# Optimization experiments

Hardware: AMD Instinct MI355X
Metric: run time of the kernel (lower is better)

Reference implementation:

```python
import jax, jax.numpy as jnp
import numpy as np

C1, CS = 512, 32
EPS = 1e-5
_HI, _HJ = np.triu_indices(CS, k=1)  # pairwise (i<j) hadamard index pairs, cs_expand = 496


def setup_inputs() -> dict:
    key = jax.random.key(0)
    ks = jax.random.split(key, 9)
    B, H, W = 16, 32, 32
    return dict(
        x=jax.random.normal(ks[0], (B, C1, H, W), jnp.float32),
        fc_w=jax.random.normal(ks[1], (C1, C1), jnp.float32) * 0.05,   # 1x1 conv kernel
        fc_b=jax.random.normal(ks[2], (C1,), jnp.float32) * 0.05,
        bn_gamma=jax.random.normal(ks[3], (C1,), jnp.float32) * 0.1 + 1.0,
        bn_beta=jax.random.normal(ks[4], (C1,), jnp.float32) * 0.1,
        bn_mean=jax.random.normal(ks[5], (C1,), jnp.float32) * 0.1,    # BN running mean
        bn_var=jax.random.uniform(ks[6], (C1,), jnp.float32) + 0.5,    # BN running var (positive)
        eva_w=jax.random.normal(ks[7], (C1, C1), jnp.float32) * 0.05,
        eva_b=jax.random.normal(ks[8], (C1,), jnp.float32) * 0.05,
    )


def reference(x, fc_w, fc_b, bn_gamma, bn_beta, bn_mean, bn_var, eva_w, eva_b):
    hi = jnp.asarray(_HI)
    hj = jnp.asarray(_HJ)
    # 1x1 conv (pointwise GEMM over channels)
    x = jnp.einsum('bchw,oc->bohw', x, fc_w) + fc_b[None, :, None, None]
    # BatchNorm2d, eval mode (running stats)
    scale = bn_gamma / jnp.sqrt(bn_var + EPS)
    x = (x - bn_mean[None, :, None, None]) * scale[None, :, None, None] + bn_beta[None, :, None, None]
    # channel evaluation logits: global avg pool -> linear
    logits = jnp.mean(x, axis=(2, 3)) @ eva_w.T + eva_b  # [B, C1]
    # top-cs channel selection and gather (eval path)
    _, idx = jax.lax.top_k(logits, CS)                    # [B, CS]
    x_sel = jax.vmap(lambda xi, ii: xi[ii])(x, idx)       # [B, CS, H, W]
    # pairwise hadamard expansion: gather-multiply over (i<j) pairs
    prod = x_sel[:, hi] * x_sel[:, hj]                    # [B, cs_expand, H, W]
    # CrossHadaNorm: per-channel standardize with batch stats, affine from
    # cross-products of norm_x affine params gathered via hadamard_i/j
    mean = jnp.mean(prod, axis=(0, 2, 3), keepdims=True)
    var = jnp.var(prod, axis=(0, 2, 3), keepdims=True)
    g = (bn_gamma[hi] * bn_gamma[hj])[None, :, None, None]
    b = (bn_beta[hi] * bn_beta[hj])[None, :, None, None]
    prod = (prod - mean) / jnp.sqrt(var + EPS) * g + b
    return jnp.concatenate([x, prod], axis=1)             # [B, c1 + cs_expand, H, W]
```

## Files before the change

kernel.cpp:

```cpp
#include <hip/hip_runtime.h>
#include <stdint.h>
#include <stddef.h>

#define B_   16
#define C1_  512
#define HW_  1024
#define CS_  32
#define CE_  496
#define CO_  1008

typedef __attribute__((ext_vector_type(8))) short short8;
typedef __attribute__((ext_vector_type(4))) short short4v;
typedef __attribute__((ext_vector_type(4))) float f32x4;

__device__ __forceinline__ short f2bf(float f) {
  unsigned u = __builtin_bit_cast(unsigned, f);
  unsigned r = (u + 0x7fffu + ((u >> 16) & 1u)) >> 16;
  return (short)(unsigned short)r;
}

__device__ __forceinline__ void gload_lds16(const void* g, void* l) {
  __builtin_amdgcn_global_load_lds(
      (const __attribute__((address_space(1))) unsigned int*)g,
      (__attribute__((address_space(3))) unsigned int*)l, 16, 0, 0);
}

__global__ __launch_bounds__(256) void prep_kernel(
    const float* __restrict__ fc_w, const float* __restrict__ fc_b,
    const float* __restrict__ bn_gamma, const float* __restrict__ bn_beta,
    const float* __restrict__ bn_mean, const float* __restrict__ bn_var,
    short* __restrict__ wbf, float* __restrict__ bs, float* __restrict__ bb) {
  int bid = blockIdx.x, tid = threadIdx.x;
  if (bid < 1024) {
    int i = bid * 256 + tid;
    wbf[i] = f2bf(fc_w[i]);
  } else {
    for (int o = tid; o < C1_; o += 256) {
      float s = bn_gamma[o] / sqrtf(bn_var[o] + 1e-5f);
      bs[o] = s;
      bb[o] = (fc_b[o] - bn_mean[o]) * s + bn_beta[o];
    }
  }
}

__global__ __launch_bounds__(256) void transpose_pool(const float* __restrict__ x,
                                                      short* __restrict__ xT,
                                                      float* __restrict__ partial) {
  __shared__ float tile[64][65];
  int bid = blockIdx.x;
  int b = bid >> 7;
  int tt = bid & 127;
  int ct = tt >> 4, pt = tt & 15;
  int c0 = ct * 64, p0 = pt * 64;
  int tid = threadIdx.x;
  int rr = tid >> 4, lc = tid & 15;
  const float* xb = x + (size_t)b * C1_ * HW_;
#pragma unroll
  for (int it = 0; it < 4; ++it) {
    int c = it * 16 + rr;
    int p4 = lc * 4;
    float4 v = *(const float4*)(xb + (size_t)(c0 + c) * HW_ + p0 + p4);
    tile[c][p4+0] = v.x; tile[c][p4+1] = v.y; tile[c][p4+2] = v.z; tile[c][p4+3] = v.w;
    float g = v.x + v.y + v.z + v.w;
    g += __shfl_down(g, 8, 16);
    g += __shfl_down(g, 4, 16);
    g += __shfl_down(g, 2, 16);
    g += __shfl_down(g, 1, 16);
    if (lc == 0) partial[((size_t)b * 16 + pt) * C1_ + c0 + c] = g;
  }
  __syncthreads();
#pragma unroll
  for (int it = 0; it < 4; ++it) {
    int p = it * 16 + rr;
    int c4 = lc * 4;
    short4v o;
    o[0] = f2bf(tile[c4+0][p]);
    o[1] = f2bf(tile[c4+1][p]);
    o[2] = f2bf(tile[c4+2][p]);
    o[3] = f2bf(tile[c4+3][p]);
    *(short4v*)(xT + (size_t)b * HW_ * C1_ + (size_t)(p0 + p) * C1_ + c0 + c4) = o;
  }
}

__global__ __launch_bounds__(64) void fc_pool_kernel(
    const float* __restrict__ partial, const float* __restrict__ fc_w,
    const float* __restrict__ bs, const float* __restrict__ bb,
    float* __restrict__ pb) {
  int b = blockIdx.x >> 3, ot = blockIdx.x & 7;
  int tid = threadIdx.x;
  __shared__ float px[512];
  for (int c = tid; c < 512; c += 64) {
    float s = 0.f;
#pragma unroll
    for (int pt = 0; pt < 16; ++pt) s += partial[((size_t)b * 16 + pt) * C1_ + c];
    px[c] = s * (1.f / 1024.f);
  }
  __syncthreads();
  int o = ot * 64 + tid;
  const float4* wr = (const float4*)(fc_w + (size_t)o * 512);
  float acc = 0.f;
#pragma unroll 8
  for (int q = 0; q < 128; ++q) {
    float4 w = wr[q];
    acc += w.x * px[q*4] + w.y * px[q*4+1] + w.z * px[q*4+2] + w.w * px[q*4+3];
  }
  pb[b * 512 + o] = acc * bs[o] + bb[o];
}

__global__ __launch_bounds__(64) void eva_kernel(
    const float* __restrict__ pb, const float* __restrict__ eva_w,
    const float* __restrict__ eva_b, float* __restrict__ logits) {
  int b = blockIdx.x >> 3, ot = blockIdx.x & 7;
  int tid = threadIdx.x;
  __shared__ float ps[512];
  for (int c = tid; c < 512; c += 64) ps[c] = pb[b * 512 + c];
  __syncthreads();
  int o = ot * 64 + tid;
  const float4* wr = (const float4*)(eva_w + (size_t)o * 512);
  float acc = 0.f;
#pragma unroll 8
  for (int q = 0; q < 128; ++q) {
    float4 w = wr[q];
    acc += w.x * ps[q*4] + w.y * ps[q*4+1] + w.z * ps[q*4+2] + w.w * ps[q*4+3];
  }
  logits[b * 512 + o] = acc + eva_b[o];
}

__global__ __launch_bounds__(64) void topk_kernel(const float* __restrict__ logits,
                                                  int* __restrict__ idx) {
  int b = blockIdx.x, lane = threadIdx.x;
  float v[8];
  int base = lane * 8;
#pragma unroll
  for (int u = 0; u < 8; ++u) v[u] = logits[b * 512 + base + u];
  for (int it = 0; it < CS_; ++it) {
    float bv = v[0]; int bu = 0;
#pragma unroll
    for (int u = 1; u < 8; ++u) if (v[u] > bv) { bv = v[u]; bu = u; }
    int bi = base + bu;
    for (int off = 32; off; off >>= 1) {
      float ov = __shfl_down(bv, off);
      int   oi = __shfl_down(bi, off);
      if (ov > bv || (ov == bv && oi < bi)) { bv = ov; bi = oi; }
    }
    bi = __shfl(bi, 0);
    if (lane == 0) idx[b * CS_ + it] = bi;
#pragma unroll
    for (int u = 0; u < 8; ++u) if (bi == base + u) v[u] = -3.4e38f;
  }
}

__global__ __launch_bounds__(256) void gemm_kernel(const short* __restrict__ W,
                                                   const short* __restrict__ XT,
                                                   const float* __restrict__ bs,
                                                   const float* __restrict__ bb,
                                                   float* __restrict__ out) {
  __shared__ short As[2][128 * 32];
  __shared__ short Bs[2][128 * 32];
  int bid = (blockIdx.x & 7) * 64 + (blockIdx.x >> 3);
  int b = bid >> 5;
  int t = bid & 31;
  int mt = t & 3, ntile = t >> 2;
  int m0 = mt * 128, n0 = ntile * 128;
  const short* Ag = W + (size_t)m0 * 512;
  const short* Bg = XT + (size_t)b * HW_ * 512 + (size_t)n0 * 512;
  int tid = threadIdx.x;
  int lane = tid & 63, wave = tid >> 6;
  int wr = wave >> 1, wc = wave & 1;
  int mrow = wr * 64, ncol = wc * 64;
  int lrow = lane & 15;
  int lk = (lane >> 4) * 8;

  f32x4 acc[4][4];
#pragma unroll
  for (int i = 0; i < 4; ++i)
#pragma unroll
    for (int j = 0; j < 4; ++j) acc[i][j] = (f32x4){0.f, 0.f, 0.f, 0.f};

#pragma unroll
  for (int it = 0; it < 2; ++it) {
    int s = it * 256 + tid;
    int r = s >> 2, q = s & 3;
    gload_lds16(Ag + (size_t)r * 512 + q * 8, &As[0][s * 8]);
    gload_lds16(Bg + (size_t)r * 512 + q * 8, &Bs[0][s * 8]);
  }
  asm volatile("s_waitcnt vmcnt(0)" ::: "memory");
  __syncthreads();

  int cur = 0;
  for (int kt = 0; kt < 16; ++kt) {
    if (kt < 15) {
      int k0 = (kt + 1) * 32;
#pragma unroll
      for (int it = 0; it < 2; ++it) {
        int s = it * 256 + tid;
        int r = s >> 2, q = s & 3;
        gload_lds16(Ag + (size_t)r * 512 + k0 + q * 8, &As[cur ^ 1][s * 8]);
        gload_lds16(Bg + (size_t)r * 512 + k0 + q * 8, &Bs[cur ^ 1][s * 8]);
      }
    }
    short8 af[4], bfv[4];
#pragma unroll
    for (int f = 0; f < 4; ++f) {
      af[f]  = *(const short8*)(&As[cur][(mrow + f * 16 + lrow) * 32 + lk]);
      bfv[f] = *(const short8*)(&Bs[cur][(ncol + f * 16 + lrow) * 32 + lk]);
    }
#pragma unroll
    for (int mf = 0; mf < 4; ++mf)
#pragma unroll
      for (int nf = 0; nf < 4; ++nf)
        acc[mf][nf] = __builtin_amdgcn_mfma_f32_16x16x32_bf16(af[mf], bfv[nf], acc[mf][nf], 0, 0, 0);
    asm volatile("s_waitcnt vmcnt(0)" ::: "memory");
    __syncthreads();
    cur ^= 1;
  }

  float* outb = out + (size_t)b * CO_ * HW_;
#pragma unroll
  for (int mf = 0; mf < 4; ++mf) {
#pragma unroll
    for (int j = 0; j < 4; ++j) {
      int o = m0 + mrow + mf * 16 + (lane >> 4) * 4 + j;
      float s = bs[o], bv = bb[o];
#pragma unroll
      for (int nf = 0; nf < 4; ++nf) {
        int p = n0 + ncol + nf * 16 + lrow;
        outb[(size_t)o * HW_ + p] = acc[mf][nf][j] * s + bv;
      }
    }
  }
}

__global__ __launch_bounds__(256) void hada_kernel(
    const int* __restrict__ idx, const float* __restrict__ bn_gamma,
    const float* __restrict__ bn_beta, float* __restrict__ out) {
  int e = blockIdx.x, tid = threadIdx.x;
  int lane = tid & 63, wave = tid >> 6;
  int i = 0, rem = e;
  while (rem >= 31 - i) { rem -= 31 - i; ++i; }
  int j = i + 1 + rem;

  __shared__ int chi[16], chj[16];
  if (tid < 16) chi[tid] = idx[tid * CS_ + i];
  else if (tid < 32) chj[tid - 16] = idx[(tid - 16) * CS_ + j];
  __syncthreads();

  f32x4 p[16];
  float s = 0.f, s2 = 0.f;
#pragma unroll
  for (int b = 0; b < 16; ++b) {
    const float4* xi = (const float4*)(out + ((size_t)b * CO_ + chi[b]) * HW_);
    const float4* xj = (const float4*)(out + ((size_t)b * CO_ + chj[b]) * HW_);
    float4 a = xi[tid], c = xj[tid];
    p[b][0] = a.x * c.x; p[b][1] = a.y * c.y; p[b][2] = a.z * c.z; p[b][3] = a.w * c.w;
    s  += p[b][0] + p[b][1] + p[b][2] + p[b][3];
    s2 += p[b][0]*p[b][0] + p[b][1]*p[b][1] + p[b][2]*p[b][2] + p[b][3]*p[b][3];
  }
  for (int off = 32; off; off >>= 1) { s += __shfl_down(s, off); s2 += __shfl_down(s2, off); }
  __shared__ float red[8];
  if (lane == 0) { red[wave] = s; red[4 + wave] = s2; }
  __syncthreads();
  float S  = red[0] + red[1] + red[2] + red[3];
  float S2 = red[4] + red[5] + red[6] + red[7];
  float mean = S * (1.f / 16384.f);
  float var  = S2 * (1.f / 16384.f) - mean * mean;
  float sc = (bn_gamma[i] * bn_gamma[j]) / sqrtf(var + 1e-5f);
  float bi_ = bn_beta[i] * bn_beta[j] - mean * sc;

#pragma unroll
  for (int b = 0; b < 16; ++b) {
    float4 r;
    r.x = p[b][0] * sc + bi_;
    r.y = p[b][1] * sc + bi_;
    r.z = p[b][2] * sc + bi_;
    r.w = p[b][3] * sc + bi_;
    ((float4*)(out + ((size_t)b * CO_ + C1_ + e) * HW_))[tid] = r;
  }
}

#define XT_OFF     ((size_t)0)
#define WBF_OFF    ((size_t)16777216)
#define PART_OFF   ((size_t)17301504)
#define PB_OFF     ((size_t)17825792)
#define LOG_OFF    ((size_t)17858560)
#define IDX_OFF    ((size_t)17891328)
#define BS_OFF     ((size_t)17893376)
#define BB_OFF     ((size_t)17895424)

extern "C" void kernel_launch(void* const* d_in, const int* in_sizes, int n_in,
                              void* d_out, int out_size, void* d_ws, size_t ws_size,
                              hipStream_t stream) {
  const float* x        = (const float*)d_in[0];
  const float* fc_w     = (const float*)d_in[1];
  const float* fc_b     = (const float*)d_in[2];
  const float* bn_gamma = (const float*)d_in[3];
  const float* bn_beta  = (const float*)d_in[4];
  const float* bn_mean  = (const float*)d_in[5];
  const float* bn_var   = (const float*)d_in[6];
  const float* eva_w    = (const float*)d_in[7];
  const float* eva_b    = (const float*)d_in[8];
  float* out = (float*)d_out;
  char* ws = (char*)d_ws;

  short* xT      = (short*)(ws + XT_OFF);
  short* wbf     = (short*)(ws + WBF_OFF);
  float* partial = (float*)(ws + PART_OFF);
  float* pb      = (float*)(ws + PB_OFF);
  float* logits  = (float*)(ws + LOG_OFF);
  int*   idx     = (int*)(ws + IDX_OFF);
  float* bs      = (float*)(ws + BS_OFF);
  float* bb      = (float*)(ws + BB_OFF);

  hipLaunchKernelGGL(prep_kernel, dim3(1025), dim3(256), 0, stream,
                     fc_w, fc_b, bn_gamma, bn_beta, bn_mean, bn_var, wbf, bs, bb);
  hipLaunchKernelGGL(transpose_pool, dim3(2048), dim3(256), 0, stream, x, xT, partial);
  hipLaunchKernelGGL(fc_pool_kernel, dim3(128), dim3(64), 0, stream,
                     partial, fc_w, bs, bb, pb);
  hipLaunchKernelGGL(eva_kernel, dim3(128), dim3(64), 0, stream,
                     pb, eva_w, eva_b, logits);
  hipLaunchKernelGGL(topk_kernel, dim3(16), dim3(64), 0, stream, logits, idx);
  hipLaunchKernelGGL(gemm_kernel, dim3(512), dim3(256), 0, stream, wbf, xT, bs, bb, out);
  hipLaunchKernelGGL(hada_kernel, dim3(CE_), dim3(256), 0, stream,
                     idx, bn_gamma, bn_beta, out);
}
```

Baseline: 96.47 us.

## Widen GEMM K-tile to 64 with XOR-swizzled LDS and staged coalesced epilogue

The GEMM kernel now loads 64-wide K tiles into a single 64KB shared buffer. The layout is XOR-swizzled to avoid LDS bank conflicts on the MFMA fragment reads, and halving the K iterations halves the barrier count. The epilogue stages each row block through LDS so the global stores become contiguous float4 writes instead of strided scalar stores. The larger LDS footprint may reduce occupancy, and the epilogue adds extra barriers.

```diff
diff --git a/kernel.cpp b/kernel.cpp
--- a/kernel.cpp
+++ b/kernel.cpp
@@ -155,8 +155,7 @@
                                                    const float* __restrict__ bs,
                                                    const float* __restrict__ bb,
                                                    float* __restrict__ out) {
-  __shared__ short As[2][128 * 32];
-  __shared__ short Bs[2][128 * 32];
+  __shared__ char smem[65536];
   int bid = (blockIdx.x & 7) * 64 + (blockIdx.x >> 3);
   int b = bid >> 5;
   int t = bid & 31;
@@ -169,7 +168,7 @@
   int wr = wave >> 1, wc = wave & 1;
   int mrow = wr * 64, ncol = wc * 64;
   int lrow = lane & 15;
-  int lk = (lane >> 4) * 8;
+  int swz = (lrow & 7) << 4;
 
   f32x4 acc[4][4];
 #pragma unroll
@@ -177,58 +176,76 @@
 #pragma unroll
     for (int j = 0; j < 4; ++j) acc[i][j] = (f32x4){0.f, 0.f, 0.f, 0.f};
 
-#pragma unroll
-  for (int it = 0; it < 2; ++it) {
-    int s = it * 256 + tid;
-    int r = s >> 2, q = s & 3;
-    gload_lds16(Ag + (size_t)r * 512 + q * 8, &As[0][s * 8]);
-    gload_lds16(Bg + (size_t)r * 512 + q * 8, &Bs[0][s * 8]);
-  }
+#define STAGE(dstbase, k0)                                                      \
+  {                                                                             \
+    _Pragma("unroll")                                                           \
+    for (int it_ = 0; it_ < 4; ++it_) {                                         \
+      int s_ = it_ * 256 + tid;                                                 \
+      int L_ = s_ * 16;                                                         \
+      int row_ = L_ >> 7;                                                       \
+      int w_ = L_ & 127;                                                        \
+      int srcs_ = (w_ ^ ((row_ & 7) << 4)) >> 1;                                \
+      gload_lds16(Ag + (size_t)row_ * 512 + (k0) + srcs_,                       \
+                  smem + (dstbase) + L_);                                       \
+      gload_lds16(Bg + (size_t)row_ * 512 + (k0) + srcs_,                       \
+                  smem + 32768 + (dstbase) + L_);                               \
+    }                                                                           \
+  }
+
+  STAGE(0, 0)
   asm volatile("s_waitcnt vmcnt(0)" ::: "memory");
   __syncthreads();
 
   int cur = 0;
-  for (int kt = 0; kt < 16; ++kt) {
-    if (kt < 15) {
-      int k0 = (kt + 1) * 32;
-#pragma unroll
-      for (int it = 0; it < 2; ++it) {
-        int s = it * 256 + tid;
-        int r = s >> 2, q = s & 3;
-        gload_lds16(Ag + (size_t)r * 512 + k0 + q * 8, &As[cur ^ 1][s * 8]);
-        gload_lds16(Bg + (size_t)r * 512 + k0 + q * 8, &Bs[cur ^ 1][s * 8]);
+  for (int kt = 0; kt < 8; ++kt) {
+    if (kt < 7) STAGE((cur ^ 1) * 16384, (kt + 1) * 64)
+    const char* Ab = smem + cur * 16384;
+    const char* Bb = smem + 32768 + cur * 16384;
+#pragma unroll
+    for (int kk = 0; kk < 2; ++kk) {
+      int kb = (kk * 64 + (lane >> 4) * 16) ^ swz;
+      short8 af[4], bfv[4];
+#pragma unroll
+      for (int f = 0; f < 4; ++f) {
+        af[f]  = *(const short8*)(Ab + (mrow + f * 16 + lrow) * 128 + kb);
+        bfv[f] = *(const short8*)(Bb + (ncol + f * 16 + lrow) * 128 + kb);
       }
+#pragma unroll
+      for (int mf = 0; mf < 4; ++mf)
+#pragma unroll
+        for (int nf = 0; nf < 4; ++nf)
+          acc[mf][nf] = __builtin_amdgcn_mfma_f32_16x16x32_bf16(af[mf], bfv[nf], acc[mf][nf], 0, 0, 0);
     }
-    short8 af[4], bfv[4];
-#pragma unroll
-    for (int f = 0; f < 4; ++f) {
-      af[f]  = *(const short8*)(&As[cur][(mrow + f * 16 + lrow) * 32 + lk]);
-      bfv[f] = *(const short8*)(&Bs[cur][(ncol + f * 16 + lrow) * 32 + lk]);
-    }
-#pragma unroll
-    for (int mf = 0; mf < 4; ++mf)
-#pragma unroll
-      for (int nf = 0; nf < 4; ++nf)
-        acc[mf][nf] = __builtin_amdgcn_mfma_f32_16x16x32_bf16(af[mf], bfv[nf], acc[mf][nf], 0, 0, 0);
     asm volatile("s_waitcnt vmcnt(0)" ::: "memory");
     __syncthreads();
     cur ^= 1;
   }
 
+  float* ldsf = (float*)smem;
   float* outb = out + (size_t)b * CO_ * HW_;
+  int lr4 = (lane >> 4) * 4;
 #pragma unroll
   for (int mf = 0; mf < 4; ++mf) {
+    __syncthreads();
 #pragma unroll
     for (int j = 0; j < 4; ++j) {
-      int o = m0 + mrow + mf * 16 + (lane >> 4) * 4 + j;
+      int o = m0 + mrow + mf * 16 + lr4 + j;
       float s = bs[o], bv = bb[o];
-#pragma unroll
-      for (int nf = 0; nf < 4; ++nf) {
-        int p = n0 + ncol + nf * 16 + lrow;
-        outb[(size_t)o * HW_ + p] = acc[mf][nf][j] * s + bv;
-      }
+      int r32 = wr * 16 + lr4 + j;
+#pragma unroll
+      for (int nf = 0; nf < 4; ++nf)
+        ldsf[r32 * 132 + ncol + nf * 16 + lrow] = acc[mf][nf][j] * s + bv;
     }
-  }
+    __syncthreads();
+    int r32 = tid >> 3, seg = tid & 7;
+    int o = m0 + mf * 16 + (r32 >> 4) * 64 + (r32 & 15);
+    float* dst = outb + (size_t)o * HW_ + n0 + seg * 16;
+    const float* srcl = &ldsf[r32 * 132 + seg * 16];
+#pragma unroll
+    for (int q = 0; q < 4; ++q)
+      *(float4*)(dst + q * 4) = *(const float4*)(srcl + q * 4);
+  }
+#undef STAGE
 }
 
 __global__ __launch_bounds__(256) void hada_kernel(
```

Result: slower. 105.5 us (+9.4%).
